# Kernel optimization log

Hardware: AMD Instinct MI355X
Metric: run time of the kernel (lower is better)

The kernel has to match this reference:

```python
import jax, jax.numpy as jnp
import numpy as np
import math

D_MODEL = 1024
NUM_HEADS = 16
HEAD_DIM = D_MODEL // NUM_HEADS


def setup_inputs() -> dict:
    key = jax.random.key(0)
    k1, k2, k3, k4 = jax.random.split(key, 4)
    x = jax.random.normal(k1, (1, 4096, D_MODEL), dtype=jnp.float32)
    # torch nn.Linear weights: [out_features, in_features]
    s = 1.0 / math.sqrt(D_MODEL)
    w_qkv = jax.random.uniform(k2, (3 * D_MODEL, D_MODEL), jnp.float32, -s, s)
    w_out = jax.random.uniform(k3, (D_MODEL, D_MODEL), jnp.float32, -s, s)
    b_out = jax.random.uniform(k4, (D_MODEL,), jnp.float32, -s, s)
    return {"x": x, "w_qkv": w_qkv, "w_out": w_out, "b_out": b_out}


def reference(x, w_qkv, w_out, b_out):
    B, T, C = x.shape
    qkv = (x @ w_qkv.T).reshape(B, T, 3, NUM_HEADS, HEAD_DIM)
    q, k, v = qkv[:, :, 0], qkv[:, :, 1], qkv[:, :, 2]  # [B,T,H,Dh]
    scores = jnp.einsum('bthd,bshd->bhts', q, k) / jnp.sqrt(jnp.float32(HEAD_DIM))
    weights = jax.nn.softmax(scores, axis=-1)  # [B,H,T,S]
    attn = jnp.einsum('bhts,bshd->bthd', weights, v).reshape(B, T, C)
    return attn @ w_out.T + b_out
```

## Files before the change

kernel.cpp:

```cpp
#include <hip/hip_runtime.h>
#include <hip/hip_bf16.h>
#include <math.h>

#define T_SEQ 4096
#define NH 16
#define HD 64
#define C_DIM 1024
#define N_QKV 3072

typedef __bf16 bf16x8 __attribute__((ext_vector_type(8)));
typedef __bf16 bf16x2 __attribute__((ext_vector_type(2)));
typedef float f32x4 __attribute__((ext_vector_type(4)));
typedef float f32x16 __attribute__((ext_vector_type(16)));
typedef unsigned short u16x8 __attribute__((ext_vector_type(8)));
typedef unsigned short u16x4 __attribute__((ext_vector_type(4)));
typedef unsigned int u32x4 __attribute__((ext_vector_type(4)));

__device__ __forceinline__ unsigned short f2bf(float f) {
  unsigned u = __builtin_bit_cast(unsigned, f);
  u += 0x7FFFu + ((u >> 16) & 1u);
  return (unsigned short)(u >> 16);
}

__device__ __forceinline__ bf16x8 lds_frag(const unsigned short* p) {
  return __builtin_bit_cast(bf16x8, *reinterpret_cast<const u16x8*>(p));
}

__global__ void convert_kernel(const float* __restrict__ x,
                               const float* __restrict__ wqkv,
                               const float* __restrict__ wout,
                               unsigned short* __restrict__ xb,
                               unsigned short* __restrict__ wqkvb,
                               unsigned short* __restrict__ woutb) {
  const int NX = T_SEQ * C_DIM;
  const int NW = N_QKV * C_DIM;
  const int NO = C_DIM * C_DIM;
  int idx = blockIdx.x * blockDim.x + threadIdx.x;
  int i = idx * 4;
  if (i >= NX + NW + NO) return;
  const float* src;
  unsigned short* dst;
  if (i < NX)            { src = x + i;                dst = xb + i; }
  else if (i < NX + NW)  { src = wqkv + (i - NX);      dst = wqkvb + (i - NX); }
  else                   { src = wout + (i - NX - NW); dst = woutb + (i - NX - NW); }
  float4 v = *reinterpret_cast<const float4*>(src);
  u16x4 o;
  o[0] = f2bf(v.x); o[1] = f2bf(v.y); o[2] = f2bf(v.z); o[3] = f2bf(v.w);
  *reinterpret_cast<u16x4*>(dst) = o;
}

template <bool F32OUT>
__global__ __launch_bounds__(256) void gemm_bt(
    const unsigned short* __restrict__ A, const unsigned short* __restrict__ Bm,
    unsigned short* __restrict__ Cb, float* __restrict__ Cf,
    const float* __restrict__ bias, int M, int N, int K,
    int scale_cols, float ascale) {
  __shared__ __align__(16) unsigned short As[128 * 64];
  __shared__ __align__(16) unsigned short Bs[128 * 64];
  const int tid = threadIdx.x;
  const int lane = tid & 63, wid = tid >> 6;
  const int l15 = lane & 15, g = lane >> 4;
  const int nbn = N >> 7;
  const int bm = blockIdx.x / nbn, bn = blockIdx.x % nbn;
  const int wm = wid >> 1, wn = wid & 1;

  f32x4 acc[4][4];
  const f32x4 zero = {0.f, 0.f, 0.f, 0.f};
#pragma unroll
  for (int m = 0; m < 4; m++)
#pragma unroll
    for (int n = 0; n < 4; n++) acc[m][n] = zero;

  for (int k0 = 0; k0 < K; k0 += 64) {
    __syncthreads();
#pragma unroll
    for (int i = 0; i < 4; i++) {
      int c = tid + i * 256;
      int row = c >> 3, slot = c & 7;
      int b_off = row * 128 + ((slot * 16) ^ ((row & 7) << 4));
      u16x8 va = *reinterpret_cast<const u16x8*>(A + (size_t)(bm * 128 + row) * K + k0 + slot * 8);
      *reinterpret_cast<u16x8*>(reinterpret_cast<char*>(As) + b_off) = va;
      u16x8 vb = *reinterpret_cast<const u16x8*>(Bm + (size_t)(bn * 128 + row) * K + k0 + slot * 8);
      *reinterpret_cast<u16x8*>(reinterpret_cast<char*>(Bs) + b_off) = vb;
    }
    __syncthreads();
#pragma unroll
    for (int kk = 0; kk < 2; kk++) {
      bf16x8 af[4], bfr[4];
#pragma unroll
      for (int m = 0; m < 4; m++) {
        int row = wm * 64 + m * 16 + l15;
        af[m] = lds_frag(reinterpret_cast<const unsigned short*>(
            reinterpret_cast<const char*>(As) + row * 128 + ((kk * 64 + g * 16) ^ ((l15 & 7) << 4))));
      }
#pragma unroll
      for (int n = 0; n < 4; n++) {
        int row = wn * 64 + n * 16 + l15;
        bfr[n] = lds_frag(reinterpret_cast<const unsigned short*>(
            reinterpret_cast<const char*>(Bs) + row * 128 + ((kk * 64 + g * 16) ^ ((l15 & 7) << 4))));
      }
#pragma unroll
      for (int m = 0; m < 4; m++)
#pragma unroll
        for (int n = 0; n < 4; n++)
          acc[m][n] = __builtin_amdgcn_mfma_f32_16x16x32_bf16(af[m], bfr[n], acc[m][n], 0, 0, 0);
    }
  }
#pragma unroll
  for (int m = 0; m < 4; m++) {
    int row0 = bm * 128 + wm * 64 + m * 16 + g * 4;
#pragma unroll
    for (int n = 0; n < 4; n++) {
      int col = bn * 128 + wn * 64 + n * 16 + l15;
      float bi = 0.f;
      if (F32OUT) bi = bias[col];
      float cs = (col < scale_cols) ? ascale : 1.0f;
#pragma unroll
      for (int r = 0; r < 4; r++) {
        float v = acc[m][n][r];
        if (F32OUT) Cf[(size_t)(row0 + r) * N + col] = v + bi;
        else        Cb[(size_t)(row0 + r) * N + col] = f2bf(v * cs);
      }
    }
  }
}

__global__ __launch_bounds__(256, 2) void attn_kernel(
    const unsigned short* __restrict__ qkv,
    unsigned short* __restrict__ attn) {
  __shared__ __align__(16) unsigned short Ksh[2][2][64 * 72];
  __shared__ __align__(16) unsigned short Vsh[2][2][64 * 72];
  const int tid = threadIdx.x;
  const int lane = tid & 63, wid = tid >> 6;
  const int qw = wid & 1, str = wid >> 1;
  const int stid = qw * 64 + lane;
  const int l31 = lane & 31, hi = lane >> 5;
  const int sw = (blockIdx.x & 7) * 64 + (blockIdx.x >> 3);
  const int h = sw >> 5;
  const int qb = sw & 31;
  const int t0 = qb * 128 + qw * 64;
  const int q = l31;
  const int kvbase = str * (T_SEQ / 2);
  const int NT = T_SEQ / 128;

  const int krow = stid >> 1, ks4 = (stid & 1) * 4;
  const int kp = stid & 31, d0 = (stid >> 5) * 16;

  bf16x8 qf[2][4];
#pragma unroll
  for (int j = 0; j < 2; j++)
#pragma unroll
    for (int ds = 0; ds < 4; ds++) {
      const unsigned short* p =
          qkv + (size_t)(t0 + j * 32 + q) * N_QKV + h * HD + ds * 16 + hi * 8;
      qf[j][ds] = __builtin_bit_cast(bf16x8, *reinterpret_cast<const u16x8*>(p));
    }

  float l_run[2] = {0.f, 0.f};
  f32x16 o[2][2];
  const f32x16 zero16 = {0.f};
  o[0][0] = zero16; o[0][1] = zero16; o[1][0] = zero16; o[1][1] = zero16;
  f32x16 minit;
#pragma unroll
  for (int i = 0; i < 16; i++) minit[i] = -4.0f;

  u16x8 kreg[4], vreg[2][2];
  {
    const int kv0 = kvbase;
#pragma unroll
    for (int i = 0; i < 4; i++)
      kreg[i] = *reinterpret_cast<const u16x8*>(
          qkv + (size_t)(kv0 + krow) * N_QKV + C_DIM + h * HD + (ks4 + i) * 8);
    const unsigned short* vsrc =
        qkv + (size_t)(kv0 + 2 * kp) * N_QKV + 2 * C_DIM + h * HD + d0;
    vreg[0][0] = *reinterpret_cast<const u16x8*>(vsrc);
    vreg[0][1] = *reinterpret_cast<const u16x8*>(vsrc + 8);
    vreg[1][0] = *reinterpret_cast<const u16x8*>(vsrc + N_QKV);
    vreg[1][1] = *reinterpret_cast<const u16x8*>(vsrc + N_QKV + 8);
  }

  for (int t = 0; t < NT; t++) {
    unsigned short* Kb = Ksh[str][t & 1];
    unsigned short* Vb = Vsh[str][t & 1];
#pragma unroll
    for (int i = 0; i < 4; i++)
      *reinterpret_cast<u16x8*>(&Kb[krow * 72 + (ks4 + i) * 8]) = kreg[i];
#pragma unroll
    for (int half = 0; half < 2; half++)
#pragma unroll
      for (int jj = 0; jj < 8; jj++) {
        int d = d0 + half * 8 + jj;
        unsigned pk = (unsigned)vreg[0][half][jj] | ((unsigned)vreg[1][half][jj] << 16);
        *reinterpret_cast<unsigned*>(&Vb[d * 72 + 2 * kp]) = pk;
      }
    if (t < NT - 1) {
      const int kv0 = kvbase + (t + 1) * 64;
#pragma unroll
      for (int i = 0; i < 4; i++)
        kreg[i] = *reinterpret_cast<const u16x8*>(
            qkv + (size_t)(kv0 + krow) * N_QKV + C_DIM + h * HD + (ks4 + i) * 8);
      const unsigned short* vsrc =
          qkv + (size_t)(kv0 + 2 * kp) * N_QKV + 2 * C_DIM + h * HD + d0;
      vreg[0][0] = *reinterpret_cast<const u16x8*>(vsrc);
      vreg[0][1] = *reinterpret_cast<const u16x8*>(vsrc + 8);
      vreg[1][0] = *reinterpret_cast<const u16x8*>(vsrc + N_QKV);
      vreg[1][1] = *reinterpret_cast<const u16x8*>(vsrc + N_QKV + 8);
    }
    __syncthreads();

    f32x16 s[2][2];
    s[0][0] = minit; s[0][1] = minit; s[1][0] = minit; s[1][1] = minit;
#pragma unroll
    for (int nt = 0; nt < 2; nt++)
#pragma unroll
      for (int ds = 0; ds < 4; ds++) {
        bf16x8 kf = lds_frag(&Kb[(nt * 32 + l31) * 72 + ds * 16 + hi * 8]);
        s[0][nt] = __builtin_amdgcn_mfma_f32_32x32x16_bf16(kf, qf[0][ds], s[0][nt], 0, 0, 0);
        s[1][nt] = __builtin_amdgcn_mfma_f32_32x32x16_bf16(kf, qf[1][ds], s[1][nt], 0, 0, 0);
      }

    unsigned wA[2][2][8];
#pragma unroll
    for (int j = 0; j < 2; j++) {
      float psum[16];
#pragma unroll
      for (int nt = 0; nt < 2; nt++)
#pragma unroll
        for (int i = 0; i < 8; i++) {
          float pa = __builtin_amdgcn_exp2f(s[j][nt][2 * i]);
          float pb = __builtin_amdgcn_exp2f(s[j][nt][2 * i + 1]);
          bf16x2 pk = {(__bf16)pa, (__bf16)pb};
          wA[j][nt][i] = __builtin_bit_cast(unsigned, pk);
          psum[nt * 8 + i] = pa + pb;
        }
#pragma unroll
      for (int i = 0; i < 8; i++) psum[i] += psum[i + 8];
#pragma unroll
      for (int i = 0; i < 4; i++) psum[i] += psum[i + 4];
      l_run[j] += (psum[0] + psum[2]) + (psum[1] + psum[3]);
    }

#pragma unroll
    for (int j = 0; j < 2; j++)
#pragma unroll
      for (int nt = 0; nt < 2; nt++)
#pragma unroll
        for (int base = 0; base < 8; base += 4)
#pragma unroll
          for (int k = 0; k < 2; k++) {
            unsigned A = wA[j][nt][base + k];
            unsigned B = wA[j][nt][base + k + 2];
            unsigned snd = hi ? A : B;
            unsigned rcv = __shfl_xor(snd, 32);
            wA[j][nt][base + k]     = hi ? rcv : A;
            wA[j][nt][base + k + 2] = hi ? B   : rcv;
          }

#pragma unroll
    for (int nt = 0; nt < 2; nt++) {
      u32x4 g00 = {wA[0][nt][0], wA[0][nt][1], wA[0][nt][2], wA[0][nt][3]};
      u32x4 g01 = {wA[0][nt][4], wA[0][nt][5], wA[0][nt][6], wA[0][nt][7]};
      u32x4 g10 = {wA[1][nt][0], wA[1][nt][1], wA[1][nt][2], wA[1][nt][3]};
      u32x4 g11 = {wA[1][nt][4], wA[1][nt][5], wA[1][nt][6], wA[1][nt][7]};
      bf16x8 pf00 = __builtin_bit_cast(bf16x8, g00);
      bf16x8 pf01 = __builtin_bit_cast(bf16x8, g01);
      bf16x8 pf10 = __builtin_bit_cast(bf16x8, g10);
      bf16x8 pf11 = __builtin_bit_cast(bf16x8, g11);
#pragma unroll
      for (int dblk = 0; dblk < 2; dblk++) {
        bf16x8 vf0 = lds_frag(&Vb[(dblk * 32 + l31) * 72 + nt * 32 + hi * 8]);
        bf16x8 vf1 = lds_frag(&Vb[(dblk * 32 + l31) * 72 + nt * 32 + 16 + hi * 8]);
        o[0][dblk] = __builtin_amdgcn_mfma_f32_32x32x16_bf16(vf0, pf00, o[0][dblk], 0, 0, 0);
        o[0][dblk] = __builtin_amdgcn_mfma_f32_32x32x16_bf16(vf1, pf01, o[0][dblk], 0, 0, 0);
        o[1][dblk] = __builtin_amdgcn_mfma_f32_32x32x16_bf16(vf0, pf10, o[1][dblk], 0, 0, 0);
        o[1][dblk] = __builtin_amdgcn_mfma_f32_32x32x16_bf16(vf1, pf11, o[1][dblk], 0, 0, 0);
      }
    }
  }

  float* ob = reinterpret_cast<float*>(&Ksh[0][0][0]);
  float* lb = reinterpret_cast<float*>(&Vsh[0][0][0]);
  const int midx = qw * 64 + lane;
#pragma unroll
  for (int j = 0; j < 2; j++) {
    __syncthreads();
    if (str == 1) {
#pragma unroll
      for (int dblk = 0; dblk < 2; dblk++)
#pragma unroll
        for (int r = 0; r < 16; r++)
          ob[(dblk * 16 + r) * 128 + midx] = o[j][dblk][r];
      lb[midx] = l_run[j];
    }
    __syncthreads();
    if (str == 0) {
#pragma unroll
      for (int dblk = 0; dblk < 2; dblk++)
#pragma unroll
        for (int r = 0; r < 16; r++)
          o[j][dblk][r] += ob[(dblk * 16 + r) * 128 + midx];
      l_run[j] += lb[midx];
    }
  }

  if (str == 0) {
#pragma unroll
    for (int j = 0; j < 2; j++) {
      float lr = l_run[j];
      float inv = 1.f / (lr + __shfl_xor(lr, 32));
      const int t = t0 + j * 32 + q;
#pragma unroll
      for (int dblk = 0; dblk < 2; dblk++)
#pragma unroll
        for (int qd = 0; qd < 4; qd++) {
          u16x4 w;
#pragma unroll
          for (int i = 0; i < 4; i++) w[i] = f2bf(o[j][dblk][qd * 4 + i] * inv);
          *reinterpret_cast<u16x4*>(
              &attn[(size_t)t * C_DIM + h * HD + dblk * 32 + qd * 8 + hi * 4]) = w;
        }
    }
  }
}

extern "C" void kernel_launch(void* const* d_in, const int* in_sizes, int n_in,
                              void* d_out, int out_size, void* d_ws, size_t ws_size,
                              hipStream_t stream) {
  const float* x     = (const float*)d_in[0];
  const float* w_qkv = (const float*)d_in[1];
  const float* w_out = (const float*)d_in[2];
  const float* b_out = (const float*)d_in[3];
  float* out = (float*)d_out;
  char* ws = (char*)d_ws;
  unsigned short* xb    = (unsigned short*)(ws);
  unsigned short* wqkvb = (unsigned short*)(ws + (8u << 20));
  unsigned short* woutb = (unsigned short*)(ws + (14u << 20));
  unsigned short* qkvb  = (unsigned short*)(ws + (16u << 20));
  unsigned short* attnb = (unsigned short*)(ws + (40u << 20));

  const float QSCALE = 0.125f * 1.44269504f;

  convert_kernel<<<8192, 256, 0, stream>>>(x, w_qkv, w_out, xb, wqkvb, woutb);
  gemm_bt<false><<<768, 256, 0, stream>>>(xb, wqkvb, qkvb, nullptr, nullptr,
                                          T_SEQ, N_QKV, C_DIM, C_DIM, QSCALE);
  attn_kernel<<<512, 256, 0, stream>>>(qkvb, attnb);
  gemm_bt<true><<<256, 256, 0, stream>>>(attnb, woutb, nullptr, out, b_out,
                                         T_SEQ, C_DIM, C_DIM, 0, 1.0f);
}
```

Measured before the change: 159.3 us.

## Use direct global-to-LDS loads in GEMM, permlane swaps and priority hints in attention

The GEMM tile loads now use global_load_lds to write straight into shared memory, with the XOR swizzle moved onto the global source column, so the register round trip is gone. The attention kernel replaces the cross-half shuffle with v_permlane32_swap, wraps its MFMA blocks in s_setprio, and moves K/V into a single shared buffer. The convert kernel becomes a grid-stride loop with fewer blocks. Together these aim to cut load latency and instruction overhead, at the cost of more subtle LDS layout and ordering assumptions.

```diff
diff --git a/kernel.cpp b/kernel.cpp
--- a/kernel.cpp
+++ b/kernel.cpp
@@ -24,6 +24,12 @@
 
 __device__ __forceinline__ bf16x8 lds_frag(const unsigned short* p) {
   return __builtin_bit_cast(bf16x8, *reinterpret_cast<const u16x8*>(p));
+}
+
+__device__ __forceinline__ void gload_lds16(const unsigned short* g, unsigned short* l) {
+  __builtin_amdgcn_global_load_lds(
+      (const __attribute__((address_space(1))) unsigned int*)(uintptr_t)(const void*)g,
+      (__attribute__((address_space(3))) unsigned int*)(uintptr_t)(void*)l, 16, 0, 0);
 }
 
 __global__ void convert_kernel(const float* __restrict__ x,
@@ -35,18 +41,20 @@
   const int NX = T_SEQ * C_DIM;
   const int NW = N_QKV * C_DIM;
   const int NO = C_DIM * C_DIM;
-  int idx = blockIdx.x * blockDim.x + threadIdx.x;
-  int i = idx * 4;
-  if (i >= NX + NW + NO) return;
-  const float* src;
-  unsigned short* dst;
-  if (i < NX)            { src = x + i;                dst = xb + i; }
-  else if (i < NX + NW)  { src = wqkv + (i - NX);      dst = wqkvb + (i - NX); }
-  else                   { src = wout + (i - NX - NW); dst = woutb + (i - NX - NW); }
-  float4 v = *reinterpret_cast<const float4*>(src);
-  u16x4 o;
-  o[0] = f2bf(v.x); o[1] = f2bf(v.y); o[2] = f2bf(v.z); o[3] = f2bf(v.w);
-  *reinterpret_cast<u16x4*>(dst) = o;
+  const int NTOT = (NX + NW + NO) / 4;
+  for (int idx = blockIdx.x * blockDim.x + threadIdx.x; idx < NTOT;
+       idx += gridDim.x * blockDim.x) {
+    int i = idx * 4;
+    const float* src;
+    unsigned short* dst;
+    if (i < NX)            { src = x + i;                dst = xb + i; }
+    else if (i < NX + NW)  { src = wqkv + (i - NX);      dst = wqkvb + (i - NX); }
+    else                   { src = wout + (i - NX - NW); dst = woutb + (i - NX - NW); }
+    float4 v = *reinterpret_cast<const float4*>(src);
+    u16x4 o;
+    o[0] = f2bf(v.x); o[1] = f2bf(v.y); o[2] = f2bf(v.z); o[3] = f2bf(v.w);
+    *reinterpret_cast<u16x4*>(dst) = o;
+  }
 }
 
 template <bool F32OUT>
@@ -77,11 +85,9 @@
     for (int i = 0; i < 4; i++) {
       int c = tid + i * 256;
       int row = c >> 3, slot = c & 7;
-      int b_off = row * 128 + ((slot * 16) ^ ((row & 7) << 4));
-      u16x8 va = *reinterpret_cast<const u16x8*>(A + (size_t)(bm * 128 + row) * K + k0 + slot * 8);
-      *reinterpret_cast<u16x8*>(reinterpret_cast<char*>(As) + b_off) = va;
-      u16x8 vb = *reinterpret_cast<const u16x8*>(Bm + (size_t)(bn * 128 + row) * K + k0 + slot * 8);
-      *reinterpret_cast<u16x8*>(reinterpret_cast<char*>(Bs) + b_off) = vb;
+      int col = slot ^ (row & 7);
+      gload_lds16(A + (size_t)(bm * 128 + row) * K + k0 + col * 8, &As[c * 8]);
+      gload_lds16(Bm + (size_t)(bn * 128 + row) * K + k0 + col * 8, &Bs[c * 8]);
     }
     __syncthreads();
 #pragma unroll
@@ -128,8 +134,7 @@
 __global__ __launch_bounds__(256, 2) void attn_kernel(
     const unsigned short* __restrict__ qkv,
     unsigned short* __restrict__ attn) {
-  __shared__ __align__(16) unsigned short Ksh[2][2][64 * 72];
-  __shared__ __align__(16) unsigned short Vsh[2][2][64 * 72];
+  __shared__ __align__(16) unsigned short smem[2 * 2 * 9216];
   const int tid = threadIdx.x;
   const int lane = tid & 63, wid = tid >> 6;
   const int qw = wid & 1, str = wid >> 1;
@@ -141,10 +146,12 @@
   const int t0 = qb * 128 + qw * 64;
   const int q = l31;
   const int kvbase = str * (T_SEQ / 2);
-  const int NT = T_SEQ / 128;
+  const int NT = (T_SEQ / 2) / 64;
+
+  unsigned short* Sbase = &smem[str * 2 * 9216];
 
   const int krow = stid >> 1, ks4 = (stid & 1) * 4;
-  const int kp = stid & 31, d0 = (stid >> 5) * 16;
+  const int kp = stid & 31, vd0 = (stid >> 5) * 16;
 
   bf16x8 qf[2][4];
 #pragma unroll
@@ -166,13 +173,12 @@
 
   u16x8 kreg[4], vreg[2][2];
   {
-    const int kv0 = kvbase;
 #pragma unroll
     for (int i = 0; i < 4; i++)
       kreg[i] = *reinterpret_cast<const u16x8*>(
-          qkv + (size_t)(kv0 + krow) * N_QKV + C_DIM + h * HD + (ks4 + i) * 8);
+          qkv + (size_t)(kvbase + krow) * N_QKV + C_DIM + h * HD + (ks4 + i) * 8);
     const unsigned short* vsrc =
-        qkv + (size_t)(kv0 + 2 * kp) * N_QKV + 2 * C_DIM + h * HD + d0;
+        qkv + (size_t)(kvbase + 2 * kp) * N_QKV + 2 * C_DIM + h * HD + vd0;
     vreg[0][0] = *reinterpret_cast<const u16x8*>(vsrc);
     vreg[0][1] = *reinterpret_cast<const u16x8*>(vsrc + 8);
     vreg[1][0] = *reinterpret_cast<const u16x8*>(vsrc + N_QKV);
@@ -180,8 +186,8 @@
   }
 
   for (int t = 0; t < NT; t++) {
-    unsigned short* Kb = Ksh[str][t & 1];
-    unsigned short* Vb = Vsh[str][t & 1];
+    unsigned short* Kb = Sbase + (t & 1) * 9216;
+    unsigned short* Vb = Kb + 4608;
 #pragma unroll
     for (int i = 0; i < 4; i++)
       *reinterpret_cast<u16x8*>(&Kb[krow * 72 + (ks4 + i) * 8]) = kreg[i];
@@ -189,7 +195,7 @@
     for (int half = 0; half < 2; half++)
 #pragma unroll
       for (int jj = 0; jj < 8; jj++) {
-        int d = d0 + half * 8 + jj;
+        int d = vd0 + half * 8 + jj;
         unsigned pk = (unsigned)vreg[0][half][jj] | ((unsigned)vreg[1][half][jj] << 16);
         *reinterpret_cast<unsigned*>(&Vb[d * 72 + 2 * kp]) = pk;
       }
@@ -200,7 +206,7 @@
         kreg[i] = *reinterpret_cast<const u16x8*>(
             qkv + (size_t)(kv0 + krow) * N_QKV + C_DIM + h * HD + (ks4 + i) * 8);
       const unsigned short* vsrc =
-          qkv + (size_t)(kv0 + 2 * kp) * N_QKV + 2 * C_DIM + h * HD + d0;
+          qkv + (size_t)(kv0 + 2 * kp) * N_QKV + 2 * C_DIM + h * HD + vd0;
       vreg[0][0] = *reinterpret_cast<const u16x8*>(vsrc);
       vreg[0][1] = *reinterpret_cast<const u16x8*>(vsrc + 8);
       vreg[1][0] = *reinterpret_cast<const u16x8*>(vsrc + N_QKV);
@@ -210,6 +216,7 @@
 
     f32x16 s[2][2];
     s[0][0] = minit; s[0][1] = minit; s[1][0] = minit; s[1][1] = minit;
+    __builtin_amdgcn_s_setprio(1);
 #pragma unroll
     for (int nt = 0; nt < 2; nt++)
 #pragma unroll
@@ -218,6 +225,7 @@
         s[0][nt] = __builtin_amdgcn_mfma_f32_32x32x16_bf16(kf, qf[0][ds], s[0][nt], 0, 0, 0);
         s[1][nt] = __builtin_amdgcn_mfma_f32_32x32x16_bf16(kf, qf[1][ds], s[1][nt], 0, 0, 0);
       }
+    __builtin_amdgcn_s_setprio(0);
 
     unsigned wA[2][2][8];
 #pragma unroll
@@ -238,10 +246,6 @@
 #pragma unroll
       for (int i = 0; i < 4; i++) psum[i] += psum[i + 4];
       l_run[j] += (psum[0] + psum[2]) + (psum[1] + psum[3]);
-    }
-
-#pragma unroll
-    for (int j = 0; j < 2; j++)
 #pragma unroll
       for (int nt = 0; nt < 2; nt++)
 #pragma unroll
@@ -250,12 +254,13 @@
           for (int k = 0; k < 2; k++) {
             unsigned A = wA[j][nt][base + k];
             unsigned B = wA[j][nt][base + k + 2];
-            unsigned snd = hi ? A : B;
-            unsigned rcv = __shfl_xor(snd, 32);
-            wA[j][nt][base + k]     = hi ? rcv : A;
-            wA[j][nt][base + k + 2] = hi ? B   : rcv;
+            asm("v_permlane32_swap_b32 %0, %1" : "+v"(A), "+v"(B));
+            wA[j][nt][base + k]     = A;
+            wA[j][nt][base + k + 2] = B;
           }
-
+    }
+
+    __builtin_amdgcn_s_setprio(1);
 #pragma unroll
     for (int nt = 0; nt < 2; nt++) {
       u32x4 g00 = {wA[0][nt][0], wA[0][nt][1], wA[0][nt][2], wA[0][nt][3]};
@@ -276,10 +281,11 @@
         o[1][dblk] = __builtin_amdgcn_mfma_f32_32x32x16_bf16(vf1, pf11, o[1][dblk], 0, 0, 0);
       }
     }
-  }
-
-  float* ob = reinterpret_cast<float*>(&Ksh[0][0][0]);
-  float* lb = reinterpret_cast<float*>(&Vsh[0][0][0]);
+    __builtin_amdgcn_s_setprio(0);
+  }
+
+  float* ob = reinterpret_cast<float*>(&smem[0]);
+  float* lb = ob + 8192;
   const int midx = qw * 64 + lane;
 #pragma unroll
   for (int j = 0; j < 2; j++) {
@@ -340,7 +346,7 @@
 
   const float QSCALE = 0.125f * 1.44269504f;
 
-  convert_kernel<<<8192, 256, 0, stream>>>(x, w_qkv, w_out, xb, wqkvb, woutb);
+  convert_kernel<<<2048, 256, 0, stream>>>(x, w_qkv, w_out, xb, wqkvb, woutb);
   gemm_bt<false><<<768, 256, 0, stream>>>(xb, wqkvb, qkvb, nullptr, nullptr,
                                           T_SEQ, N_QKV, C_DIM, C_DIM, QSCALE);
   attn_kernel<<<512, 256, 0, stream>>>(qkvb, attnb);
```

After: 185.7 us. +16.5%, slower.
